# Optimization experiments

Hardware: AMD Instinct MI355X
Metric: run time of the kernel (lower is better)

The kernel has to match this reference:

```python
import jax, jax.numpy as jnp
import numpy as np

NUM_HEADS = 16


def _qdq(x):
    """Symmetric int8 fake-quant along the last axis (per-token for
    activations, per-output-channel for [out,in] weights). Equivalent math to
    int8 GEMM with dynamic scales: (x_q @ w_q.T) * sx * sw == qdq(x) @ qdq(w).T."""
    s = jnp.maximum(jnp.max(jnp.abs(x), axis=-1, keepdims=True) / 127.0, 1e-8)
    return jnp.clip(jnp.round(x / s), -127.0, 127.0) * s


def setup_inputs() -> dict:
    key = jax.random.key(0)
    ks = jax.random.split(key, 8)
    B, N, M, D = 2, 4096, 512, 2048
    w_std = 0.02
    return {
        "x": jax.random.normal(ks[0], (B, N, D), jnp.float32),
        "cond": jax.random.normal(ks[1], (B, M, D), jnp.float32),
        "wq": jax.random.normal(ks[2], (D, D), jnp.float32) * w_std,
        "bq": jax.random.normal(ks[3], (D,), jnp.float32) * w_std,
        "wkv": jax.random.normal(ks[4], (2 * D, D), jnp.float32) * w_std,
        "bkv": jax.random.normal(ks[5], (2 * D,), jnp.float32) * w_std,
        "wp": jax.random.normal(ks[6], (D, D), jnp.float32) * w_std,
        "bp": jax.random.normal(ks[7], (D,), jnp.float32) * w_std,
    }


def reference(x, cond, wq, bq, wkv, bkv, wp, bp):
    B, N, C = x.shape
    M = cond.shape[1]
    H = NUM_HEADS
    Dh = C // H

    # W8A8 dynamic-scale q projection (per-token act quant, per-channel weight quant)
    q = _qdq(x) @ _qdq(wq).T + bq                      # [B,N,C]
    # fp16-style kv projection
    kv = cond @ wkv.T + bkv                            # [B,M,2C]
    k, v = jnp.split(kv, 2, axis=-1)                   # view(...,2,H,Dh).unbind(2)

    q = q.reshape(B, N, H, Dh)
    k = k.reshape(B, M, H, Dh)
    v = v.reshape(B, M, H, Dh)

    scale = 1.0 / np.sqrt(Dh)
    attn = jax.nn.softmax(jnp.einsum('bnhd,bmhd->bhnm', q, k) * scale, axis=-1)
    o = jnp.einsum('bhnm,bmhd->bnhd', attn, v).reshape(B, N, C)

    # fused quant_sum (per-token requant of attention output) + W8A8 proj
    out = _qdq(o) @ _qdq(wp).T + bp                    # [B,N,C]
    return out
```

## Files before the change

kernel.cpp:

```cpp
#include <hip/hip_runtime.h>
#include <cstdint>
#include <cstddef>


typedef __bf16 bf16_t;
typedef __bf16 bf16x8 __attribute__((ext_vector_type(8)));
typedef float f32x4 __attribute__((ext_vector_type(4)));

__device__ __forceinline__ void gld16(void* lds, const void* g) {
    __builtin_amdgcn_global_load_lds(
        (__attribute__((address_space(1))) uint32_t*)(uintptr_t)g,
        (__attribute__((address_space(3))) uint32_t*)(uint32_t)(uintptr_t)lds,
        16, 0, 0);
}

__device__ __forceinline__ void load8(const float* p, int i, float* v) {
    const float4* p4 = (const float4*)p;
    float4 a = p4[2 * i], b = p4[2 * i + 1];
    v[0] = a.x; v[1] = a.y; v[2] = a.z; v[3] = a.w;
    v[4] = b.x; v[5] = b.y; v[6] = b.z; v[7] = b.w;
}
__device__ __forceinline__ void load8(const bf16_t* p, int i, float* v) {
    bf16x8 t = ((const bf16x8*)p)[i];
#pragma unroll
    for (int j = 0; j < 8; ++j) v[j] = (float)t[j];
}

template <int QUANT, typename T>
__global__ __launch_bounds__(256) void rowpack(const T* __restrict__ in,
                                               bf16_t* __restrict__ out, int K) {
    const int tid = threadIdx.x;
    const size_t row = blockIdx.x;
    const T* rp = in + row * (size_t)K;
    const int n8 = K >> 3;
    float scale = 1.0f;
    if (QUANT) {
        float m = 0.f;
        for (int i = tid; i < n8; i += 256) {
            float v[8];
            load8(rp, i, v);
#pragma unroll
            for (int j = 0; j < 8; ++j) m = fmaxf(m, fabsf(v[j]));
        }
        __shared__ float red[256];
        red[tid] = m;
        __syncthreads();
        for (int s = 128; s > 0; s >>= 1) {
            if (tid < s) red[tid] = fmaxf(red[tid], red[tid + s]);
            __syncthreads();
        }
        scale = fmaxf(red[0] * (1.0f / 127.0f), 1e-8f);
    }
    const int KT = K >> 5;
    const int p = (int)(row >> 7), c = ((int)row >> 4) & 7, lm = (int)row & 15;
    for (int i = tid; i < n8; i += 256) {
        const int col = i << 3;
        const int kt = col >> 5, quad = (col >> 3) & 3;
        float v[8];
        load8(rp, i, v);
        bf16x8 o8;
#pragma unroll
        for (int j = 0; j < 8; ++j) {
            float q = v[j];
            if (QUANT) {
                q = rintf(q / scale);
                q = fminf(127.f, fmaxf(-127.f, q)) * scale;
            }
            o8[j] = (bf16_t)q;
        }
        const size_t dst = ((size_t)(p * KT + kt) * 8 + c) * 512 + (quad * 16 + lm) * 8;
        *(bf16x8*)(out + dst) = o8;
    }
}

template <int MODE>
__device__ __forceinline__ void epi_store(void* C, int N, int row, int col, float v) {
    if (MODE == 1) {
        ((float*)C)[(size_t)row * N + col] = v;
    } else if (MODE == 0) {
        const int b = row >> 12, n = row & 4095;
        const int h = col >> 7, d = col & 127;
        const int p = n >> 6, mt = (n >> 4) & 3, lmq = n & 15;
        const int kq = d >> 5, qq = (d >> 3) & 3, jq = d & 7;
        const size_t idx = (((size_t)(b * 16 + h) * 64 + p) * 16 + kq * 4 + mt) * 512 +
                           (qq * 16 + lmq) * 8 + jq;
        ((bf16_t*)C)[idx] = (bf16_t)v;
    } else {
        const int b = row >> 9, m = row & 511;
        const int half = col >> 11, h = (col >> 7) & 15, d = col & 127;
        const int t8 = m >> 6;
        bf16_t* out = (bf16_t*)C;
        if (half == 0) {
            const int nt = (m >> 4) & 3, lmk = m & 15;
            const int kc = d >> 5, qk = (d >> 3) & 3, jk = d & 7;
            const size_t idx = (((size_t)(b * 16 + h) * 8 + t8) * 16 + kc * 4 + nt) * 512 +
                               (qk * 16 + lmk) * 8 + jk;
            out[idx] = (bf16_t)v;
        } else {
            const int kv2 = (m >> 5) & 1, qv = (m >> 3) & 3, jv = m & 7;
            const int ntv = d >> 4, lmv = d & 15;
            const size_t idx = 2097152 +
                (((size_t)(b * 16 + h) * 8 + t8) * 16 + kv2 * 8 + ntv) * 512 +
                (qv * 16 + lmv) * 8 + jv;
            out[idx] = (bf16_t)v;
        }
    }
}

template <int MODE>
__global__ __launch_bounds__(256) void gemm_pk(const bf16_t* __restrict__ A,
                                               const bf16_t* __restrict__ B,
                                               const float* __restrict__ bias,
                                               void* __restrict__ C,
                                               int N, int K) {
    __shared__ __align__(16) bf16_t sA[8192];
    __shared__ __align__(16) bf16_t sB[8192];

    const int tid = threadIdx.x;
    const int l = tid & 63, w = tid >> 6;
    const int lm = l & 15, quad = l >> 4;
    const int wm = w & 1, wn = w >> 1;
    const int KT = K >> 5;
    const size_t aBase = (size_t)blockIdx.y * KT * 8 * 512;
    const size_t bBase = (size_t)blockIdx.x * KT * 8 * 512;

    f32x4 acc[4][4] = {};
    const int NIT = K >> 6;
    for (int kt = 0; kt < NIT; ++kt) {
        __syncthreads();
#pragma unroll
        for (int it = 0; it < 4; ++it) {
            const int c = it * 4 + w;
            gld16(sA + c * 512, A + aBase + ((size_t)kt * 16 + c) * 512 + l * 8);
            gld16(sB + c * 512, B + bBase + ((size_t)kt * 16 + c) * 512 + l * 8);
        }
        __syncthreads();
#pragma unroll
        for (int h = 0; h < 2; ++h) {
            bf16x8 af[4], bfr[4];
#pragma unroll
            for (int i = 0; i < 4; ++i)
                af[i] = *(const bf16x8*)(sA + (h * 8 + wm * 4 + i) * 512 + l * 8);
#pragma unroll
            for (int j = 0; j < 4; ++j)
                bfr[j] = *(const bf16x8*)(sB + (h * 8 + wn * 4 + j) * 512 + l * 8);
#pragma unroll
            for (int i = 0; i < 4; ++i)
#pragma unroll
                for (int j = 0; j < 4; ++j)
                    acc[i][j] =
                        __builtin_amdgcn_mfma_f32_16x16x32_bf16(af[i], bfr[j], acc[i][j], 0, 0, 0);
        }
    }
#pragma unroll
    for (int i = 0; i < 4; ++i) {
#pragma unroll
        for (int j = 0; j < 4; ++j) {
            const int col = blockIdx.x * 128 + wn * 64 + j * 16 + lm;
            const float bv = bias[col];
#pragma unroll
            for (int r = 0; r < 4; ++r) {
                const int row = blockIdx.y * 128 + wm * 64 + i * 16 + quad * 4 + r;
                epi_store<MODE>(C, N, row, col, acc[i][j][r] + bv);
            }
        }
    }
}

__global__ __launch_bounds__(256) void gemm_kv(const bf16_t* __restrict__ A,
                                               const bf16_t* __restrict__ B,
                                               const float* __restrict__ bias,
                                               bf16_t* __restrict__ C,
                                               int N, int K) {
    __shared__ __align__(16) bf16_t sA[4096];
    __shared__ __align__(16) bf16_t sB[8192];

    const int tid = threadIdx.x;
    const int l = tid & 63, w = tid >> 6;
    const int lm = l & 15, quad = l >> 4;
    const int wm = w & 1, wn = w >> 1;
    const int KT = K >> 5;
    const int p = blockIdx.y >> 1, hh = blockIdx.y & 1;
    const size_t aPan = (size_t)p * KT * 8 * 512;
    const size_t bBase = (size_t)blockIdx.x * KT * 8 * 512;

    f32x4 acc[2][4] = {};
    const int NIT = K >> 6;
    for (int kt = 0; kt < NIT; ++kt) {
        __syncthreads();
#pragma unroll
        for (int it = 0; it < 2; ++it) {
            const int lc = it * 4 + w;
            const int s = lc >> 2, cc = lc & 3;
            gld16(sA + lc * 512,
                  A + aPan + ((size_t)(kt * 2 + s) * 8 + hh * 4 + cc) * 512 + l * 8);
        }
#pragma unroll
        for (int it = 0; it < 4; ++it) {
            const int lc = it * 4 + w;
            gld16(sB + lc * 512, B + bBase + ((size_t)kt * 16 + lc) * 512 + l * 8);
        }
        __syncthreads();
#pragma unroll
        for (int s = 0; s < 2; ++s) {
            bf16x8 af[2], bfr[4];
#pragma unroll
            for (int i = 0; i < 2; ++i)
                af[i] = *(const bf16x8*)(sA + (s * 4 + wm * 2 + i) * 512 + l * 8);
#pragma unroll
            for (int j = 0; j < 4; ++j)
                bfr[j] = *(const bf16x8*)(sB + (s * 8 + wn * 4 + j) * 512 + l * 8);
#pragma unroll
            for (int i = 0; i < 2; ++i)
#pragma unroll
                for (int j = 0; j < 4; ++j)
                    acc[i][j] =
                        __builtin_amdgcn_mfma_f32_16x16x32_bf16(af[i], bfr[j], acc[i][j], 0, 0, 0);
        }
    }
#pragma unroll
    for (int i = 0; i < 2; ++i) {
#pragma unroll
        for (int j = 0; j < 4; ++j) {
            const int col = blockIdx.x * 128 + wn * 64 + j * 16 + lm;
            const float bv = bias[col];
#pragma unroll
            for (int r = 0; r < 4; ++r) {
                const int row = blockIdx.y * 64 + wm * 32 + i * 16 + quad * 4 + r;
                epi_store<2>(C, N, row, col, acc[i][j][r] + bv);
            }
        }
    }
}

__global__ __launch_bounds__(256, 2) void attn64(const bf16_t* __restrict__ qpk,
                                                 const bf16_t* __restrict__ kvpk,
                                                 bf16_t* __restrict__ o) {
    constexpr float SCALE = 0.08838834764831845f;
    __shared__ __align__(16) bf16_t sQP[8192];
    __shared__ __align__(16) bf16_t sKV[16384];
    __shared__ float redM[4][64];
    __shared__ float redS[4][64];

    const int tid = threadIdx.x;
    const int l = tid & 63, w = tid >> 6;
    const int lm = l & 15, quad = l >> 4;
    const int b = blockIdx.z, h = blockIdx.y;
    const int p = blockIdx.x;
    const int bh = b * 16 + h;
    const size_t qbase = ((size_t)bh * 64 + p) * 8192;
    const size_t kbase = (size_t)bh * 65536;
    const size_t vbase = 2097152 + (size_t)bh * 65536;

#pragma unroll
    for (int it = 0; it < 4; ++it) {
        const int c = it * 4 + w;
        gld16(sQP + c * 512, qpk + qbase + (size_t)c * 512 + l * 8);
    }

    f32x4 sfr[8][4] = {};
#pragma unroll
    for (int g = 0; g < 4; ++g) {
        __syncthreads();
#pragma unroll
        for (int it = 0; it < 8; ++it) {
            const int c = it * 4 + w;
            gld16(sKV + c * 512, kvpk + kbase + ((size_t)g * 32 + c) * 512 + l * 8);
        }
        __syncthreads();
#pragma unroll
        for (int kc = 0; kc < 4; ++kc) {
#pragma unroll
            for (int kk = 0; kk < 2; ++kk) {
                bf16x8 bb = *(const bf16x8*)(sKV + (kk * 16 + kc * 4 + w) * 512 + l * 8);
#pragma unroll
                for (int mt = 0; mt < 4; ++mt) {
                    bf16x8 aa = *(const bf16x8*)(sQP + (kc * 4 + mt) * 512 + l * 8);
                    sfr[g * 2 + kk][mt] =
                        __builtin_amdgcn_mfma_f32_16x16x32_bf16(aa, bb, sfr[g * 2 + kk][mt], 0, 0, 0);
                }
            }
        }
    }

    float inv[4][4];
    {
        float mymax[4][4];
#pragma unroll
        for (int mt = 0; mt < 4; ++mt)
#pragma unroll
            for (int r = 0; r < 4; ++r) {
                float m = -3.0e38f;
#pragma unroll
                for (int t8 = 0; t8 < 8; ++t8) m = fmaxf(m, sfr[t8][mt][r]);
                m = fmaxf(m, __shfl_xor(m, 1));
                m = fmaxf(m, __shfl_xor(m, 2));
                m = fmaxf(m, __shfl_xor(m, 4));
                m = fmaxf(m, __shfl_xor(m, 8));
                mymax[mt][r] = m;
            }
        if (lm == 0) {
#pragma unroll
            for (int mt = 0; mt < 4; ++mt)
#pragma unroll
                for (int r = 0; r < 4; ++r)
                    redM[w][mt * 16 + quad * 4 + r] = mymax[mt][r];
        }
        __syncthreads();
#pragma unroll
        for (int mt = 0; mt < 4; ++mt)
#pragma unroll
            for (int r = 0; r < 4; ++r) {
                const int row = mt * 16 + quad * 4 + r;
                const float M =
                    fmaxf(fmaxf(redM[0][row], redM[1][row]), fmaxf(redM[2][row], redM[3][row])) *
                    SCALE;
                float s = 0.f;
#pragma unroll
                for (int t8 = 0; t8 < 8; ++t8) {
                    const float pe = __expf(sfr[t8][mt][r] * SCALE - M);
                    sfr[t8][mt][r] = pe;
                    s += pe;
                }
                s += __shfl_xor(s, 1);
                s += __shfl_xor(s, 2);
                s += __shfl_xor(s, 4);
                s += __shfl_xor(s, 8);
                if (lm == 0) redS[w][row] = s;
            }
        __syncthreads();
#pragma unroll
        for (int mt = 0; mt < 4; ++mt)
#pragma unroll
            for (int r = 0; r < 4; ++r) {
                const int row = mt * 16 + quad * 4 + r;
                inv[mt][r] = 1.f / (redS[0][row] + redS[1][row] + redS[2][row] + redS[3][row]);
            }
    }

    f32x4 oc[4][2] = {};
    const int ktd = w >> 1;
    const int quadd = (w & 1) * 2 + (lm >> 3);
    const int jd = lm & 7;
#pragma unroll
    for (int g = 0; g < 4; ++g) {
        __syncthreads();
#pragma unroll
        for (int kk = 0; kk < 2; ++kk)
#pragma unroll
            for (int mt = 0; mt < 4; ++mt)
#pragma unroll
                for (int r = 0; r < 4; ++r)
                    sQP[(mt * 4 + kk * 2 + ktd) * 512 + (quadd * 16 + quad * 4 + r) * 8 + jd] =
                        (bf16_t)sfr[g * 2 + kk][mt][r];
#pragma unroll
        for (int it = 0; it < 8; ++it) {
            const int c = it * 4 + w;
            gld16(sKV + c * 512, kvpk + vbase + ((size_t)g * 32 + c) * 512 + l * 8);
        }
        __syncthreads();
#pragma unroll
        for (int kvf = 0; kvf < 4; ++kvf) {
            const int kk = kvf >> 1, kv2 = kvf & 1;
            bf16x8 aa[4];
#pragma unroll
            for (int mt = 0; mt < 4; ++mt)
                aa[mt] = *(const bf16x8*)(sQP + (mt * 4 + kvf) * 512 + l * 8);
#pragma unroll
            for (int ni = 0; ni < 2; ++ni) {
                bf16x8 bb =
                    *(const bf16x8*)(sKV + (kk * 16 + kv2 * 8 + w * 2 + ni) * 512 + l * 8);
#pragma unroll
                for (int mt = 0; mt < 4; ++mt)
                    oc[mt][ni] =
                        __builtin_amdgcn_mfma_f32_16x16x32_bf16(aa[mt], bb, oc[mt][ni], 0, 0, 0);
            }
        }
    }

#pragma unroll
    for (int mt = 0; mt < 4; ++mt)
#pragma unroll
        for (int ni = 0; ni < 2; ++ni)
#pragma unroll
            for (int r = 0; r < 4; ++r) {
                const int row = mt * 16 + quad * 4 + r;
                const int d = w * 32 + ni * 16 + lm;
                o[((size_t)b * 4096 + p * 64 + row) * 2048 + h * 128 + d] =
                    (bf16_t)(oc[mt][ni][r] * inv[mt][r]);
            }
}

extern "C" void kernel_launch(void* const* d_in, const int* in_sizes, int n_in,
                              void* d_out, int out_size, void* d_ws, size_t ws_size,
                              hipStream_t stream) {
    (void)in_sizes; (void)n_in; (void)out_size; (void)ws_size;
    const float* x    = (const float*)d_in[0];
    const float* cond = (const float*)d_in[1];
    const float* wq   = (const float*)d_in[2];
    const float* bq   = (const float*)d_in[3];
    const float* wkv  = (const float*)d_in[4];
    const float* bkv  = (const float*)d_in[5];
    const float* wp   = (const float*)d_in[6];
    const float* bp   = (const float*)d_in[7];

    const size_t MB = 1ull << 20;
    uint8_t* ws = (uint8_t*)d_ws;
    bf16_t* qxpk   = (bf16_t*)(ws + 0);
    bf16_t* qpk    = (bf16_t*)(ws + 32 * MB);
    bf16_t* wqpk   = (bf16_t*)(ws + 64 * MB);
    bf16_t* wkvpk  = (bf16_t*)(ws + 72 * MB);
    bf16_t* wppk   = (bf16_t*)(ws + 88 * MB);
    bf16_t* condpk = (bf16_t*)(ws + 96 * MB);
    bf16_t* kvpk   = (bf16_t*)(ws + 100 * MB);
    bf16_t* o_nat  = qxpk;
    bf16_t* opk    = qpk;

    dim3 blk(256);
    rowpack<1, float><<<8192, blk, 0, stream>>>(x, qxpk, 2048);
    rowpack<1, float><<<2048, blk, 0, stream>>>(wq, wqpk, 2048);
    rowpack<1, float><<<2048, blk, 0, stream>>>(wp, wppk, 2048);
    rowpack<0, float><<<1024, blk, 0, stream>>>(cond, condpk, 2048);
    rowpack<0, float><<<4096, blk, 0, stream>>>(wkv, wkvpk, 2048);
    gemm_pk<0><<<dim3(16, 64), blk, 0, stream>>>(qxpk, wqpk, bq, qpk, 2048, 2048);
    gemm_kv<<<dim3(32, 16), blk, 0, stream>>>(condpk, wkvpk, bkv, kvpk, 4096, 2048);
    attn64<<<dim3(64, 16, 2), blk, 0, stream>>>(qpk, kvpk, o_nat);
    rowpack<1, bf16_t><<<8192, blk, 0, stream>>>(o_nat, opk, 2048);
    gemm_pk<1><<<dim3(16, 64), blk, 0, stream>>>(opk, wppk, bp, (float*)d_out, 2048, 2048);
}
```

Baseline: 537.5 us.

## Replace packed GEMM with 256x256 double-buffered 8-wave kernel and swizzled grid

Replaces the 128x128 single-buffered packed GEMM used for the q and output projections with a 512-thread kernel that computes 256x256 tiles. It double-buffers 64-deep K slices in LDS so global loads for tile t+2 run during MFMA work. It also interleaves LDS fragment reads with MFMA phases using explicit barriers, setprio and waitcnt, and remaps block IDs so neighbouring workgroups share operand panels. The aims are better data reuse per tile, hiding load latency and improving L2 locality, at the cost of 128 KB of LDS, one workgroup per CU, and only 256 workgroups to cover the GPU.

```diff
diff --git a/kernel.cpp b/kernel.cpp
--- a/kernel.cpp
+++ b/kernel.cpp
@@ -107,60 +107,146 @@
     }
 }
 
+__device__ __forceinline__ void stage_tile256(const bf16_t* __restrict__ A,
+                                              const bf16_t* __restrict__ B,
+                                              bf16_t* sa, bf16_t* sb,
+                                              int pa, int pb, int KT, int t,
+                                              int w, int l) {
+#pragma unroll
+    for (int it = 0; it < 4; ++it) {
+        const int ci = w * 4 + it;
+        const int h = ci >> 4, kt2 = (ci >> 3) & 1, c = ci & 7;
+        const size_t ga = (((size_t)(pa + h) * KT + (2 * t + kt2)) * 8 + c) * 512 + l * 8;
+        const size_t gb = (((size_t)(pb + h) * KT + (2 * t + kt2)) * 8 + c) * 512 + l * 8;
+        gld16(sa + ci * 512, A + ga);
+        gld16(sb + ci * 512, B + gb);
+    }
+}
+
 template <int MODE>
-__global__ __launch_bounds__(256) void gemm_pk(const bf16_t* __restrict__ A,
-                                               const bf16_t* __restrict__ B,
-                                               const float* __restrict__ bias,
-                                               void* __restrict__ C,
-                                               int N, int K) {
-    __shared__ __align__(16) bf16_t sA[8192];
-    __shared__ __align__(16) bf16_t sB[8192];
+__global__ __launch_bounds__(512, 1) void gemm_pk8(const bf16_t* __restrict__ A,
+                                                   const bf16_t* __restrict__ B,
+                                                   const float* __restrict__ bias,
+                                                   void* __restrict__ C,
+                                                   int N, int K) {
+    __shared__ __align__(16) bf16_t sA[2][16384];
+    __shared__ __align__(16) bf16_t sB[2][16384];
 
     const int tid = threadIdx.x;
     const int l = tid & 63, w = tid >> 6;
     const int lm = l & 15, quad = l >> 4;
     const int wm = w & 1, wn = w >> 1;
+
+    const int nwg = gridDim.x;
+    const int bid = blockIdx.x;
+    const int s = (bid & 7) * (nwg >> 3) + (bid >> 3);
+    const int bx = s & 7, by = s >> 3;
+
     const int KT = K >> 5;
-    const size_t aBase = (size_t)blockIdx.y * KT * 8 * 512;
-    const size_t bBase = (size_t)blockIdx.x * KT * 8 * 512;
-
-    f32x4 acc[4][4] = {};
-    const int NIT = K >> 6;
-    for (int kt = 0; kt < NIT; ++kt) {
-        __syncthreads();
-#pragma unroll
-        for (int it = 0; it < 4; ++it) {
-            const int c = it * 4 + w;
-            gld16(sA + c * 512, A + aBase + ((size_t)kt * 16 + c) * 512 + l * 8);
-            gld16(sB + c * 512, B + bBase + ((size_t)kt * 16 + c) * 512 + l * 8);
-        }
-        __syncthreads();
-#pragma unroll
-        for (int h = 0; h < 2; ++h) {
-            bf16x8 af[4], bfr[4];
-#pragma unroll
-            for (int i = 0; i < 4; ++i)
-                af[i] = *(const bf16x8*)(sA + (h * 8 + wm * 4 + i) * 512 + l * 8);
+    const int NT = K >> 6;
+    const int pa = by * 2, pb = bx * 2;
+
+    stage_tile256(A, B, sA[0], sB[0], pa, pb, KT, 0, w, l);
+    __builtin_amdgcn_sched_barrier(0);
+    stage_tile256(A, B, sA[1], sB[1], pa, pb, KT, 1, w, l);
+    asm volatile("s_waitcnt vmcnt(8)" ::: "memory");
+    __builtin_amdgcn_s_barrier();
+
+    f32x4 acc[8][4] = {};
+
+    for (int t = 0; t < NT; ++t) {
+        const bf16_t* sa = sA[t & 1];
+        const bf16_t* sb = sB[t & 1];
+        bf16x8 bfr[4][2];
+        bf16x8 af[2][2];
+
+#pragma unroll
+        for (int j = 0; j < 4; ++j)
+#pragma unroll
+            for (int k2 = 0; k2 < 2; ++k2)
+                bfr[j][k2] = *(const bf16x8*)(
+                    sb + ((((wn >> 1) * 2 + k2) * 8 + (wn & 1) * 4 + j) * 512) + l * 8);
+#pragma unroll
+        for (int ii = 0; ii < 2; ++ii)
+#pragma unroll
+            for (int k2 = 0; k2 < 2; ++k2)
+                af[ii][k2] = *(const bf16x8*)(sa + (((wm * 2 + k2) * 8 + ii) * 512) + l * 8);
+        __builtin_amdgcn_s_barrier();
+        asm volatile("s_waitcnt lgkmcnt(0)" ::: "memory");
+        __builtin_amdgcn_sched_barrier(0);
+        __builtin_amdgcn_s_setprio(1);
+#pragma unroll
+        for (int ii = 0; ii < 2; ++ii)
 #pragma unroll
             for (int j = 0; j < 4; ++j)
-                bfr[j] = *(const bf16x8*)(sB + (h * 8 + wn * 4 + j) * 512 + l * 8);
-#pragma unroll
-            for (int i = 0; i < 4; ++i)
+#pragma unroll
+                for (int k2 = 0; k2 < 2; ++k2)
+                    acc[ii][j] = __builtin_amdgcn_mfma_f32_16x16x32_bf16(
+                        af[ii][k2], bfr[j][k2], acc[ii][j], 0, 0, 0);
+        __builtin_amdgcn_s_setprio(0);
+        __builtin_amdgcn_s_barrier();
+
+#pragma unroll
+        for (int q = 1; q <= 2; ++q) {
+#pragma unroll
+            for (int ii = 0; ii < 2; ++ii)
+#pragma unroll
+                for (int k2 = 0; k2 < 2; ++k2)
+                    af[ii][k2] = *(const bf16x8*)(
+                        sa + (((wm * 2 + k2) * 8 + (q * 2 + ii)) * 512) + l * 8);
+            __builtin_amdgcn_s_barrier();
+            asm volatile("s_waitcnt lgkmcnt(0)" ::: "memory");
+            __builtin_amdgcn_sched_barrier(0);
+            __builtin_amdgcn_s_setprio(1);
+#pragma unroll
+            for (int ii = 0; ii < 2; ++ii)
 #pragma unroll
                 for (int j = 0; j < 4; ++j)
-                    acc[i][j] =
-                        __builtin_amdgcn_mfma_f32_16x16x32_bf16(af[i], bfr[j], acc[i][j], 0, 0, 0);
-        }
-    }
-#pragma unroll
-    for (int i = 0; i < 4; ++i) {
+#pragma unroll
+                    for (int k2 = 0; k2 < 2; ++k2)
+                        acc[q * 2 + ii][j] = __builtin_amdgcn_mfma_f32_16x16x32_bf16(
+                            af[ii][k2], bfr[j][k2], acc[q * 2 + ii][j], 0, 0, 0);
+            __builtin_amdgcn_s_setprio(0);
+            __builtin_amdgcn_s_barrier();
+        }
+
+#pragma unroll
+        for (int ii = 0; ii < 2; ++ii)
+#pragma unroll
+            for (int k2 = 0; k2 < 2; ++k2)
+                af[ii][k2] = *(const bf16x8*)(
+                    sa + (((wm * 2 + k2) * 8 + (6 + ii)) * 512) + l * 8);
+        asm volatile("s_waitcnt lgkmcnt(0)" ::: "memory");
+        __builtin_amdgcn_s_barrier();
+        if (t + 2 < NT)
+            stage_tile256(A, B, sA[t & 1], sB[t & 1], pa, pb, KT, t + 2, w, l);
+        __builtin_amdgcn_sched_barrier(0);
+        __builtin_amdgcn_s_setprio(1);
+#pragma unroll
+        for (int ii = 0; ii < 2; ++ii)
+#pragma unroll
+            for (int j = 0; j < 4; ++j)
+#pragma unroll
+                for (int k2 = 0; k2 < 2; ++k2)
+                    acc[6 + ii][j] = __builtin_amdgcn_mfma_f32_16x16x32_bf16(
+                        af[ii][k2], bfr[j][k2], acc[6 + ii][j], 0, 0, 0);
+        __builtin_amdgcn_s_setprio(0);
+        if (t + 2 < NT)
+            asm volatile("s_waitcnt vmcnt(8)" ::: "memory");
+        else
+            asm volatile("s_waitcnt vmcnt(0)" ::: "memory");
+        __builtin_amdgcn_s_barrier();
+    }
+
+#pragma unroll
+    for (int i = 0; i < 8; ++i) {
 #pragma unroll
         for (int j = 0; j < 4; ++j) {
-            const int col = blockIdx.x * 128 + wn * 64 + j * 16 + lm;
+            const int col = bx * 256 + wn * 64 + j * 16 + lm;
             const float bv = bias[col];
 #pragma unroll
             for (int r = 0; r < 4; ++r) {
-                const int row = blockIdx.y * 128 + wm * 64 + i * 16 + quad * 4 + r;
+                const int row = by * 256 + wm * 128 + i * 16 + quad * 4 + r;
                 epi_store<MODE>(C, N, row, col, acc[i][j][r] + bv);
             }
         }
@@ -422,9 +508,9 @@
     rowpack<1, float><<<2048, blk, 0, stream>>>(wp, wppk, 2048);
     rowpack<0, float><<<1024, blk, 0, stream>>>(cond, condpk, 2048);
     rowpack<0, float><<<4096, blk, 0, stream>>>(wkv, wkvpk, 2048);
-    gemm_pk<0><<<dim3(16, 64), blk, 0, stream>>>(qxpk, wqpk, bq, qpk, 2048, 2048);
+    gemm_pk8<0><<<dim3(256), dim3(512), 0, stream>>>(qxpk, wqpk, bq, qpk, 2048, 2048);
     gemm_kv<<<dim3(32, 16), blk, 0, stream>>>(condpk, wkvpk, bkv, kvpk, 4096, 2048);
     attn64<<<dim3(64, 16, 2), blk, 0, stream>>>(qpk, kvpk, o_nat);
     rowpack<1, bf16_t><<<8192, blk, 0, stream>>>(o_nat, opk, 2048);
-    gemm_pk<1><<<dim3(16, 64), blk, 0, stream>>>(opk, wppk, bp, (float*)d_out, 2048, 2048);
-}
+    gemm_pk8<1><<<dim3(256), dim3(512), 0, stream>>>(opk, wppk, bp, (float*)d_out, 2048, 2048);
+}
```

New measurement: 511.1 us. 4.9% less time.
